# Performance work log

Measured on AMD Instinct MI355X. Metric: run time of the kernel, lower is better.

Reference implementation:

```python
import jax, jax.numpy as jnp
import numpy as np


def setup_inputs() -> dict:
    key = jax.random.key(0)
    ks = jax.random.split(key, 5)
    B, C, H, W = 4, 256, 64, 64
    Cq = C // 8
    x = jax.random.normal(ks[0], (B, C, H, W), dtype=jnp.float32)
    Wq = jax.random.normal(ks[1], (Cq, C), dtype=jnp.float32) * (1.0 / np.sqrt(C))
    Wk = jax.random.normal(ks[2], (Cq, C), dtype=jnp.float32) * (1.0 / np.sqrt(C))
    Wv = jax.random.normal(ks[3], (C, C), dtype=jnp.float32) * (1.0 / np.sqrt(C))
    bq = jnp.zeros((Cq,), dtype=jnp.float32)
    bk = jnp.zeros((Cq,), dtype=jnp.float32)
    bv = jnp.zeros((C,), dtype=jnp.float32)
    gamma = jnp.ones((1,), dtype=jnp.float32)
    return {"x": x, "Wq": Wq, "bq": bq, "Wk": Wk, "bk": bk, "Wv": Wv, "bv": bv, "gamma": gamma}


def reference(x, Wq, bq, Wk, bk, Wv, bv, gamma):
    B, C, H, W = x.shape
    N = H * W
    xf = x.reshape(B, C, N)                      # (B, C, N)
    # 1x1 convs == per-pixel linear projections over channels
    q = jnp.einsum('dc,bcn->bdn', Wq, xf) + bq[None, :, None]   # (B, C/8, N)
    k = jnp.einsum('dc,bcn->bdn', Wk, xf) + bk[None, :, None]   # (B, C/8, N)
    v = jnp.einsum('dc,bcn->bdn', Wv, xf) + bv[None, :, None]   # (B, C,   N)
    # attention: note original has NO 1/sqrt(d) scaling
    scores = jnp.einsum('bdn,bdm->bnm', q, k)     # (B, N, N)
    attn = jax.nn.softmax(scores, axis=-1)
    out = jnp.einsum('bnm,bdm->bnd', attn, v)     # (B, N, C)
    out = out.transpose(0, 2, 1).reshape(B, C, H, W)
    return gamma * out + x
```

## Files before the change

### kernel.cpp

```cpp
#include <hip/hip_runtime.h>

#define BATCH 4
#define CH    256
#define DQ    32
#define NPIX  4096

typedef unsigned short u16;
typedef unsigned int   u32;
typedef __attribute__((ext_vector_type(8))) short short8;
typedef __attribute__((ext_vector_type(16))) float f32x16;

__device__ __forceinline__ float b2f(u32 u) {
  union { u32 i; float f; } v; v.i = (u & 0xffffu) << 16; return v.f;
}
__device__ __forceinline__ u16 f2b(float f) {
  union { float f; u32 i; } v; v.f = f;
  u32 x = v.i; x += 0x7fffu + ((x >> 16) & 1u);
  return (u16)(x >> 16);
}

__global__ __launch_bounds__(256) void proj(
    const float* __restrict__ x,
    const float* __restrict__ Wq, const float* __restrict__ bq,
    const float* __restrict__ Wk, const float* __restrict__ bk,
    const float* __restrict__ Wv, const float* __restrict__ bv,
    u16* __restrict__ q_t, u16* __restrict__ k_t, u16* __restrict__ v_swz)
{
  const int nt = blockIdx.x, jt = blockIdx.y, b = blockIdx.z;
  const int t = threadIdx.x;
  const int w = t >> 6, lane = t & 63, hl = lane >> 5, l31 = lane & 31;
  const int n0 = nt * 128;

  __shared__ u16 wls[2][16 * 2 * 32 * 8];
  __shared__ u16 xls[2][128 * 24];
  __shared__ float bias_s[32];

  const float* Wsrc; const float* bsrc; int jrow0;
  if (jt == 0)      { Wsrc = Wq; bsrc = bq; jrow0 = 0; }
  else if (jt == 1) { Wsrc = Wk; bsrc = bk; jrow0 = 0; }
  else              { Wsrc = Wv; bsrc = bv; jrow0 = (jt - 2) * 32; }

  for (int i = 0; i < 32; ++i) {
    const int flat = i * 256 + t;
    const int j = flat >> 8, e = flat & 255;
    const float v = Wsrc[(size_t)(jrow0 + j) * CH + e];
    const u16 hi = f2b(v);
    const u16 lo = f2b(v - b2f(hi));
    const int idx = (((e >> 4) * 2 + ((e >> 3) & 1)) * 32 + j) * 8 + (e & 7);
    wls[0][idx] = hi; wls[1][idx] = lo;
  }
  if (t < 32) bias_s[t] = bsrc[jrow0 + t];

  f32x16 acc;
  #pragma unroll
  for (int r = 0; r < 16; ++r) acc[r] = 0.f;

  const int nn = t & 127, esub = (t >> 7) * 8;
  for (int kk = 0; kk < 16; ++kk) {
    __syncthreads();
    #pragma unroll
    for (int i2 = 0; i2 < 4; ++i2) {
      const int el = esub + 2 * i2;
      const float v0 = x[((size_t)b * CH + kk * 16 + el    ) * NPIX + n0 + nn];
      const float v1 = x[((size_t)b * CH + kk * 16 + el + 1) * NPIX + n0 + nn];
      const u16 h0 = f2b(v0), h1 = f2b(v1);
      const u16 lo0 = f2b(v0 - b2f(h0)), lo1 = f2b(v1 - b2f(h1));
      *(u32*)&xls[0][nn * 24 + el] = (u32)h0 | ((u32)h1 << 16);
      *(u32*)&xls[1][nn * 24 + el] = (u32)lo0 | ((u32)lo1 << 16);
    }
    __syncthreads();
    const short8 wa_h = *(const short8*)&wls[0][((kk * 2 + hl) * 32 + l31) * 8];
    const short8 wa_l = *(const short8*)&wls[1][((kk * 2 + hl) * 32 + l31) * 8];
    const int nb = w * 32 + l31;
    const short8 xb_h = *(const short8*)&xls[0][nb * 24 + hl * 8];
    const short8 xb_l = *(const short8*)&xls[1][nb * 24 + hl * 8];
    acc = __builtin_amdgcn_mfma_f32_32x32x16_bf16(wa_h, xb_h, acc, 0, 0, 0);
    acc = __builtin_amdgcn_mfma_f32_32x32x16_bf16(wa_h, xb_l, acc, 0, 0, 0);
    acc = __builtin_amdgcn_mfma_f32_32x32x16_bf16(wa_l, xb_h, acc, 0, 0, 0);
  }

  #pragma unroll
  for (int r = 0; r < 16; ++r)
    acc[r] += bias_s[(r & 3) + 8 * (r >> 2) + 4 * hl];

  if (jt <= 1) {
    u16* dst = (jt == 0) ? q_t : k_t;
    const int n = n0 + w * 32 + l31;
    #pragma unroll
    for (int r2 = 0; r2 < 4; ++r2) {
      uint2 pk;
      pk.x = (u32)f2b(acc[4 * r2 + 0]) | ((u32)f2b(acc[4 * r2 + 1]) << 16);
      pk.y = (u32)f2b(acc[4 * r2 + 2]) | ((u32)f2b(acc[4 * r2 + 3]) << 16);
      *(uint2*)(dst + ((size_t)b * NPIX + n) * DQ + 4 * hl + 8 * r2) = pk;
    }
  } else {
    const int mc = nt * 4 + w;
    const int kc = (l31 >> 4) & 1, h3 = (l31 >> 3) & 1, j8 = l31 & 7;
    u16* dst = v_swz + (((((size_t)b * 128 + mc) * 8 + (jt - 2)) * 2 + kc) * 2 + h3) * 256 + j8;
    #pragma unroll
    for (int r = 0; r < 16; ++r) {
      const int c5 = (r & 3) + 8 * (r >> 2) + 4 * hl;
      dst[c5 * 8] = f2b(acc[r]);
    }
  }
}

__global__ __launch_bounds__(256, 2) void attn(
    const u16* __restrict__ q_t, const u16* __restrict__ k_t,
    const u16* __restrict__ v_swz, const float* __restrict__ x,
    const float* __restrict__ gamma, float* __restrict__ out)
{
  const int b = blockIdx.y, t = threadIdx.x;
  const int w = t >> 6, lane = t & 63, hl = lane >> 5, l31 = lane & 31;
  const int n0 = blockIdx.x * 32;

  __shared__ float cbuf[8192];
  __shared__ float lbuf[4][64];

  short8 qf[2];
  #pragma unroll
  for (int kd = 0; kd < 2; ++kd)
    qf[kd] = *(const short8*)(q_t + ((size_t)b * NPIX + n0 + l31) * DQ + kd * 16 + hl * 8);

  f32x16 acc[8];
  #pragma unroll
  for (int ct = 0; ct < 8; ++ct)
    #pragma unroll
    for (int r = 0; r < 16; ++r) acc[ct][r] = 0.f;
  float lrun = 0.f;

  for (int cc = 0; cc < 32; ++cc) {
    const int mc = w * 32 + cc;

    const short8 kf0 = *(const short8*)(k_t + ((size_t)b * NPIX + mc * 32 + l31) * DQ + hl * 8);
    const short8 kf1 = *(const short8*)(k_t + ((size_t)b * NPIX + mc * 32 + l31) * DQ + 16 + hl * 8);
    f32x16 st;
    #pragma unroll
    for (int r = 0; r < 16; ++r) st[r] = 0.f;
    st = __builtin_amdgcn_mfma_f32_32x32x16_bf16(kf0, qf[0], st, 0, 0, 0);
    st = __builtin_amdgcn_mfma_f32_32x32x16_bf16(kf1, qf[1], st, 0, 0, 0);

    u32 pk[4][2];
    #pragma unroll
    for (int g = 0; g < 4; ++g) {
      const float e0 = __expf(st[4 * g + 0]);
      const float e1 = __expf(st[4 * g + 1]);
      const float e2 = __expf(st[4 * g + 2]);
      const float e3 = __expf(st[4 * g + 3]);
      lrun += (e0 + e1) + (e2 + e3);
      pk[g][0] = (u32)f2b(e0) | ((u32)f2b(e1) << 16);
      pk[g][1] = (u32)f2b(e2) | ((u32)f2b(e3) << 16);
    }

    const size_t vbase = ((size_t)b * 128 + mc) * 8192;
    #pragma unroll
    for (int kc = 0; kc < 2; ++kc) {
      const u32 s0 = hl ? pk[2 * kc][0] : pk[2 * kc + 1][0];
      const u32 s1 = hl ? pk[2 * kc][1] : pk[2 * kc + 1][1];
      const u32 r0 = (u32)__shfl_xor((int)s0, 32);
      const u32 r1 = (u32)__shfl_xor((int)s1, 32);
      union { uint4 u; short8 s; } bu;
      bu.u.x = hl ? r0 : pk[2 * kc][0];
      bu.u.y = hl ? r1 : pk[2 * kc][1];
      bu.u.z = hl ? pk[2 * kc + 1][0] : r0;
      bu.u.w = hl ? pk[2 * kc + 1][1] : r1;
      #pragma unroll
      for (int ct = 0; ct < 8; ++ct) {
        const short8 av = *(const short8*)(v_swz + vbase + (size_t)(((ct * 2 + kc) * 2 + hl) * 256) + l31 * 8);
        acc[ct] = __builtin_amdgcn_mfma_f32_32x32x16_bf16(av, bu.s, acc[ct], 0, 0, 0);
      }
    }
  }

  lbuf[w][lane] = lrun;
  __syncthreads();
  for (int src = 1; src < 4; ++src) {
    if (w == src) {
      #pragma unroll
      for (int ct = 0; ct < 8; ++ct)
        #pragma unroll
        for (int r = 0; r < 16; ++r)
          cbuf[(ct * 16 + r) * 64 + lane] = acc[ct][r];
    }
    __syncthreads();
    if (w == 0) {
      #pragma unroll
      for (int ct = 0; ct < 8; ++ct)
        #pragma unroll
        for (int r = 0; r < 16; ++r)
          acc[ct][r] += cbuf[(ct * 16 + r) * 64 + lane];
    }
    __syncthreads();
  }

  if (w == 0) {
    float l = (lbuf[0][lane] + lbuf[1][lane]) + (lbuf[2][lane] + lbuf[3][lane]);
    l += __shfl_xor(l, 32);
    const float linv = 1.0f / l;
    const float g = gamma[0];
    #pragma unroll
    for (int ct = 0; ct < 8; ++ct)
      #pragma unroll
      for (int r = 0; r < 16; ++r) {
        const int c = ct * 32 + (r & 3) + 8 * (r >> 2) + 4 * hl;
        const size_t idx = ((size_t)b * CH + c) * NPIX + n0 + l31;
        out[idx] = g * acc[ct][r] * linv + x[idx];
      }
  }
}

extern "C" void kernel_launch(void* const* d_in, const int* in_sizes, int n_in,
                              void* d_out, int out_size, void* d_ws, size_t ws_size,
                              hipStream_t stream) {
  const float* x  = (const float*)d_in[0];
  const float* Wq = (const float*)d_in[1];
  const float* bq = (const float*)d_in[2];
  const float* Wk = (const float*)d_in[3];
  const float* bk = (const float*)d_in[4];
  const float* Wv = (const float*)d_in[5];
  const float* bv = (const float*)d_in[6];
  const float* gm = (const float*)d_in[7];
  float* out = (float*)d_out;

  const size_t qk_elems = (size_t)BATCH * NPIX * DQ;
  const size_t v_elems  = (size_t)BATCH * NPIX * CH;
  const size_t need = (2 * qk_elems + v_elems) * sizeof(u16);
  if (ws_size < need) return;

  u16* q_t   = (u16*)d_ws;
  u16* k_t   = q_t + qk_elems;
  u16* v_swz = k_t + qk_elems;

  proj<<<dim3(32, 10, BATCH), 256, 0, stream>>>(x, Wq, bq, Wk, bk, Wv, bv, q_t, k_t, v_swz);
  attn<<<dim3(NPIX / 32, BATCH), 256, 0, stream>>>(q_t, k_t, v_swz, x, gm, out);
}
```

Baseline: 162.5 us.

## Precompute split-bf16 weights and x tiles, pipeline QK scores in attention loop

Weight hi/lo bf16 splitting moves into a one-off wprep kernel writing to device globals, and x is pre-split and transposed by a new xprep kernel into the output buffer as scratch. The projection kernel then reads MFMA-ready fragments straight from global with no LDS or barriers, and uses two accumulators. The attention loop computes the next chunk's scores while exponentiating the current one, prefetches K two steps ahead, folds log2e into Wq so exp2 can be used, swaps halves with permlane32_swap, and raises wave priority around the PV MFMAs. The extra kernel launches and the round trip of x through global memory add traffic and launch overhead.

```diff
diff --git a/kernel.cpp b/kernel.cpp
--- a/kernel.cpp
+++ b/kernel.cpp
@@ -4,12 +4,16 @@
 #define CH    256
 #define DQ    32
 #define NPIX  4096
+#define LOG2E 1.44269504088896340736f
 
 typedef unsigned short u16;
 typedef unsigned int   u32;
 typedef __attribute__((ext_vector_type(8))) short short8;
 typedef __attribute__((ext_vector_type(16))) float f32x16;
 
+__device__ __align__(16) u16 g_wbf[10 * 2 * 8192];
+__device__ float g_bias[10 * 32];
+
 __device__ __forceinline__ float b2f(u32 u) {
   union { u32 i; float f; } v; v.i = (u & 0xffffu) << 16; return v.f;
 }
@@ -18,79 +22,133 @@
   u32 x = v.i; x += 0x7fffu + ((x >> 16) & 1u);
   return (u16)(x >> 16);
 }
-
-__global__ __launch_bounds__(256) void proj(
-    const float* __restrict__ x,
+__device__ __forceinline__ float fexp2(float x) {
+#if __has_builtin(__builtin_amdgcn_exp2f)
+  return __builtin_amdgcn_exp2f(x);
+#else
+  return __expf(x * 0.69314718055994530942f);
+#endif
+}
+
+__device__ __forceinline__ void half_swap(u32 a0, u32 a1, u32 b0, u32 b1,
+                                          int hl, uint4& o) {
+#if __has_builtin(__builtin_amdgcn_permlane32_swap)
+  const auto r0 = __builtin_amdgcn_permlane32_swap((int)a0, (int)b0, false, false);
+  const auto r1 = __builtin_amdgcn_permlane32_swap((int)a1, (int)b1, false, false);
+  o.x = (u32)r0[0]; o.y = (u32)r1[0]; o.z = (u32)r0[1]; o.w = (u32)r1[1];
+#else
+  const u32 s0 = hl ? a0 : b0;
+  const u32 s1 = hl ? a1 : b1;
+  const u32 r0 = (u32)__shfl_xor((int)s0, 32);
+  const u32 r1 = (u32)__shfl_xor((int)s1, 32);
+  o.x = hl ? r0 : a0; o.y = hl ? r1 : a1;
+  o.z = hl ? b0 : r0; o.w = hl ? b1 : r1;
+#endif
+}
+
+__global__ __launch_bounds__(256) void wprep(
     const float* __restrict__ Wq, const float* __restrict__ bq,
     const float* __restrict__ Wk, const float* __restrict__ bk,
-    const float* __restrict__ Wv, const float* __restrict__ bv,
+    const float* __restrict__ Wv, const float* __restrict__ bv)
+{
+  const int jt = blockIdx.x, t = threadIdx.x;
+  const float* Wsrc; const float* bsrc; int jrow0; float scale = 1.f;
+  if (jt == 0)      { Wsrc = Wq; bsrc = bq; jrow0 = 0; scale = LOG2E; }
+  else if (jt == 1) { Wsrc = Wk; bsrc = bk; jrow0 = 0; }
+  else              { Wsrc = Wv; bsrc = bv; jrow0 = (jt - 2) * 32; }
+
+  u16* wdst = g_wbf + (size_t)jt * 16384;
+  for (int i = 0; i < 32; ++i) {
+    const int flat = i * 256 + t;
+    const int j = flat >> 8, e = flat & 255;
+    const float v = Wsrc[(size_t)(jrow0 + j) * CH + e] * scale;
+    const u16 hi = f2b(v);
+    const u16 lo = f2b(v - b2f(hi));
+    const int idx = (((e >> 4) * 2 + ((e >> 3) & 1)) * 32 + j) * 8 + (e & 7);
+    wdst[idx] = hi; wdst[8192 + idx] = lo;
+  }
+  if (t < 32) g_bias[jt * 32 + t] = bsrc[jrow0 + t] * scale;
+}
+
+__global__ __launch_bounds__(256) void xprep(
+    const float* __restrict__ x, u16* __restrict__ xt_hi, u16* __restrict__ xt_lo)
+{
+  const int nt = blockIdx.x, kb4 = blockIdx.y * 4, b = blockIdx.z;
+  const int n0 = nt * 128, c0 = blockIdx.y * 64;
+  const int t = threadIdx.x;
+  __shared__ u32 xls[64][129];
+
+  const int tn = t & 127, cp = t >> 7;
+  for (int i = 0; i < 32; ++i) {
+    const int c = cp + 2 * i;
+    const float v = x[((size_t)b * CH + c0 + c) * NPIX + n0 + tn];
+    const u16 h = f2b(v);
+    const u16 l = f2b(v - b2f(h));
+    xls[c][tn] = (u32)h | ((u32)l << 16);
+  }
+  __syncthreads();
+
+  for (int rep = 0; rep < 4; ++rep) {
+    const int id = t + 256 * rep;
+    const int kkhl = id >> 7, n = id & 127;
+    union { short8 s; uint4 u; } vh, vl;
+    #pragma unroll
+    for (int j = 0; j < 8; ++j) {
+      const u32 p = xls[kkhl * 8 + j][n];
+      vh.s[j] = (short)(p & 0xffffu);
+      vl.s[j] = (short)(p >> 16);
+    }
+    const size_t o = ((((size_t)(b * 32 + nt) * 16 + kb4 + (kkhl >> 1)) * 2
+                       + (kkhl & 1)) * 128 + n) * 8;
+    *(uint4*)(xt_hi + o) = vh.u;
+    *(uint4*)(xt_lo + o) = vl.u;
+  }
+}
+
+__global__ __launch_bounds__(256, 4) void proj(
+    const u16* __restrict__ xt_hi, const u16* __restrict__ xt_lo,
     u16* __restrict__ q_t, u16* __restrict__ k_t, u16* __restrict__ v_swz)
 {
   const int nt = blockIdx.x, jt = blockIdx.y, b = blockIdx.z;
   const int t = threadIdx.x;
   const int w = t >> 6, lane = t & 63, hl = lane >> 5, l31 = lane & 31;
-  const int n0 = nt * 128;
-
-  __shared__ u16 wls[2][16 * 2 * 32 * 8];
-  __shared__ u16 xls[2][128 * 24];
-  __shared__ float bias_s[32];
-
-  const float* Wsrc; const float* bsrc; int jrow0;
-  if (jt == 0)      { Wsrc = Wq; bsrc = bq; jrow0 = 0; }
-  else if (jt == 1) { Wsrc = Wk; bsrc = bk; jrow0 = 0; }
-  else              { Wsrc = Wv; bsrc = bv; jrow0 = (jt - 2) * 32; }
-
-  for (int i = 0; i < 32; ++i) {
-    const int flat = i * 256 + t;
-    const int j = flat >> 8, e = flat & 255;
-    const float v = Wsrc[(size_t)(jrow0 + j) * CH + e];
-    const u16 hi = f2b(v);
-    const u16 lo = f2b(v - b2f(hi));
-    const int idx = (((e >> 4) * 2 + ((e >> 3) & 1)) * 32 + j) * 8 + (e & 7);
-    wls[0][idx] = hi; wls[1][idx] = lo;
-  }
-  if (t < 32) bias_s[t] = bsrc[jrow0 + t];
-
-  f32x16 acc;
-  #pragma unroll
-  for (int r = 0; r < 16; ++r) acc[r] = 0.f;
-
-  const int nn = t & 127, esub = (t >> 7) * 8;
+  const int nb = w * 32 + l31, n = nt * 128 + nb;
+
+  const u16* __restrict__ wb = g_wbf + (size_t)jt * 16384;
+  const size_t xtile = (size_t)(b * 32 + nt) * 16 * 2 * 128 * 8;
+  const u16* __restrict__ xh = xt_hi + xtile;
+  const u16* __restrict__ xl = xt_lo + xtile;
+
+  f32x16 acc1, acc2;
+  #pragma unroll
+  for (int r = 0; r < 16; ++r) { acc1[r] = 0.f; acc2[r] = 0.f; }
+
+  #pragma unroll
   for (int kk = 0; kk < 16; ++kk) {
-    __syncthreads();
-    #pragma unroll
-    for (int i2 = 0; i2 < 4; ++i2) {
-      const int el = esub + 2 * i2;
-      const float v0 = x[((size_t)b * CH + kk * 16 + el    ) * NPIX + n0 + nn];
-      const float v1 = x[((size_t)b * CH + kk * 16 + el + 1) * NPIX + n0 + nn];
-      const u16 h0 = f2b(v0), h1 = f2b(v1);
-      const u16 lo0 = f2b(v0 - b2f(h0)), lo1 = f2b(v1 - b2f(h1));
-      *(u32*)&xls[0][nn * 24 + el] = (u32)h0 | ((u32)h1 << 16);
-      *(u32*)&xls[1][nn * 24 + el] = (u32)lo0 | ((u32)lo1 << 16);
-    }
-    __syncthreads();
-    const short8 wa_h = *(const short8*)&wls[0][((kk * 2 + hl) * 32 + l31) * 8];
-    const short8 wa_l = *(const short8*)&wls[1][((kk * 2 + hl) * 32 + l31) * 8];
-    const int nb = w * 32 + l31;
-    const short8 xb_h = *(const short8*)&xls[0][nb * 24 + hl * 8];
-    const short8 xb_l = *(const short8*)&xls[1][nb * 24 + hl * 8];
-    acc = __builtin_amdgcn_mfma_f32_32x32x16_bf16(wa_h, xb_h, acc, 0, 0, 0);
-    acc = __builtin_amdgcn_mfma_f32_32x32x16_bf16(wa_h, xb_l, acc, 0, 0, 0);
-    acc = __builtin_amdgcn_mfma_f32_32x32x16_bf16(wa_l, xb_h, acc, 0, 0, 0);
-  }
-
+    const int aoff = ((kk * 2 + hl) * 32 + l31) * 8;
+    const short8 wah = *(const short8*)(wb + aoff);
+    const short8 wal = *(const short8*)(wb + 8192 + aoff);
+    const int boff = ((kk * 2 + hl) * 128 + nb) * 8;
+    const short8 xbh = *(const short8*)(xh + boff);
+    const short8 xbl = *(const short8*)(xl + boff);
+    acc1 = __builtin_amdgcn_mfma_f32_32x32x16_bf16(wah, xbh, acc1, 0, 0, 0);
+    acc2 = __builtin_amdgcn_mfma_f32_32x32x16_bf16(wah, xbl, acc2, 0, 0, 0);
+    acc2 = __builtin_amdgcn_mfma_f32_32x32x16_bf16(wal, xbh, acc2, 0, 0, 0);
+  }
+
+  f32x16 accv;
   #pragma unroll
   for (int r = 0; r < 16; ++r)
-    acc[r] += bias_s[(r & 3) + 8 * (r >> 2) + 4 * hl];
+    accv[r] = acc1[r] + acc2[r]
+            + g_bias[jt * 32 + (r & 3) + 8 * (r >> 2) + 4 * hl];
 
   if (jt <= 1) {
     u16* dst = (jt == 0) ? q_t : k_t;
-    const int n = n0 + w * 32 + l31;
     #pragma unroll
     for (int r2 = 0; r2 < 4; ++r2) {
       uint2 pk;
-      pk.x = (u32)f2b(acc[4 * r2 + 0]) | ((u32)f2b(acc[4 * r2 + 1]) << 16);
-      pk.y = (u32)f2b(acc[4 * r2 + 2]) | ((u32)f2b(acc[4 * r2 + 3]) << 16);
+      pk.x = (u32)f2b(accv[4 * r2 + 0]) | ((u32)f2b(accv[4 * r2 + 1]) << 16);
+      pk.y = (u32)f2b(accv[4 * r2 + 2]) | ((u32)f2b(accv[4 * r2 + 3]) << 16);
       *(uint2*)(dst + ((size_t)b * NPIX + n) * DQ + 4 * hl + 8 * r2) = pk;
     }
   } else {
@@ -100,7 +158,7 @@
     #pragma unroll
     for (int r = 0; r < 16; ++r) {
       const int c5 = (r & 3) + 8 * (r >> 2) + 4 * hl;
-      dst[c5 * 8] = f2b(acc[r]);
+      dst[c5 * 8] = f2b(accv[r]);
     }
   }
 }
@@ -129,46 +187,57 @@
     for (int r = 0; r < 16; ++r) acc[ct][r] = 0.f;
   float lrun = 0.f;
 
+  const u16* __restrict__ kb = k_t + (size_t)b * NPIX * DQ;
+
+  short8 kf0 = *(const short8*)(kb + ((w * 32) * 32 + l31) * DQ + hl * 8);
+  short8 kf1 = *(const short8*)(kb + ((w * 32) * 32 + l31) * DQ + 16 + hl * 8);
+  f32x16 st;
+  #pragma unroll
+  for (int r = 0; r < 16; ++r) st[r] = 0.f;
+  st = __builtin_amdgcn_mfma_f32_32x32x16_bf16(kf0, qf[0], st, 0, 0, 0);
+  st = __builtin_amdgcn_mfma_f32_32x32x16_bf16(kf1, qf[1], st, 0, 0, 0);
+  kf0 = *(const short8*)(kb + ((w * 32 + 1) * 32 + l31) * DQ + hl * 8);
+  kf1 = *(const short8*)(kb + ((w * 32 + 1) * 32 + l31) * DQ + 16 + hl * 8);
+
+  #pragma unroll 1
   for (int cc = 0; cc < 32; ++cc) {
     const int mc = w * 32 + cc;
-
-    const short8 kf0 = *(const short8*)(k_t + ((size_t)b * NPIX + mc * 32 + l31) * DQ + hl * 8);
-    const short8 kf1 = *(const short8*)(k_t + ((size_t)b * NPIX + mc * 32 + l31) * DQ + 16 + hl * 8);
-    f32x16 st;
+    const size_t vbase = ((size_t)b * 128 + mc) * 8192;
+
+    u32 pk[4][2];
+    #pragma unroll
+    for (int g = 0; g < 4; ++g) {
+      const float e0 = fexp2(st[4 * g + 0]);
+      const float e1 = fexp2(st[4 * g + 1]);
+      const float e2 = fexp2(st[4 * g + 2]);
+      const float e3 = fexp2(st[4 * g + 3]);
+      lrun += (e0 + e1) + (e2 + e3);
+      pk[g][0] = (u32)f2b(e0) | ((u32)f2b(e1) << 16);
+      pk[g][1] = (u32)f2b(e2) | ((u32)f2b(e3) << 16);
+    }
+
     #pragma unroll
     for (int r = 0; r < 16; ++r) st[r] = 0.f;
     st = __builtin_amdgcn_mfma_f32_32x32x16_bf16(kf0, qf[0], st, 0, 0, 0);
     st = __builtin_amdgcn_mfma_f32_32x32x16_bf16(kf1, qf[1], st, 0, 0, 0);
 
-    u32 pk[4][2];
-    #pragma unroll
-    for (int g = 0; g < 4; ++g) {
-      const float e0 = __expf(st[4 * g + 0]);
-      const float e1 = __expf(st[4 * g + 1]);
-      const float e2 = __expf(st[4 * g + 2]);
-      const float e3 = __expf(st[4 * g + 3]);
-      lrun += (e0 + e1) + (e2 + e3);
-      pk[g][0] = (u32)f2b(e0) | ((u32)f2b(e1) << 16);
-      pk[g][1] = (u32)f2b(e2) | ((u32)f2b(e3) << 16);
-    }
-
-    const size_t vbase = ((size_t)b * 128 + mc) * 8192;
+    {
+      const int mcp = w * 32 + ((cc < 30) ? cc + 2 : 31);
+      kf0 = *(const short8*)(kb + (mcp * 32 + l31) * DQ + hl * 8);
+      kf1 = *(const short8*)(kb + (mcp * 32 + l31) * DQ + 16 + hl * 8);
+    }
+
     #pragma unroll
     for (int kc = 0; kc < 2; ++kc) {
-      const u32 s0 = hl ? pk[2 * kc][0] : pk[2 * kc + 1][0];
-      const u32 s1 = hl ? pk[2 * kc][1] : pk[2 * kc + 1][1];
-      const u32 r0 = (u32)__shfl_xor((int)s0, 32);
-      const u32 r1 = (u32)__shfl_xor((int)s1, 32);
       union { uint4 u; short8 s; } bu;
-      bu.u.x = hl ? r0 : pk[2 * kc][0];
-      bu.u.y = hl ? r1 : pk[2 * kc][1];
-      bu.u.z = hl ? pk[2 * kc + 1][0] : r0;
-      bu.u.w = hl ? pk[2 * kc + 1][1] : r1;
+      half_swap(pk[2 * kc][0], pk[2 * kc][1], pk[2 * kc + 1][0], pk[2 * kc + 1][1], hl, bu.u);
+      __builtin_amdgcn_s_setprio(1);
       #pragma unroll
       for (int ct = 0; ct < 8; ++ct) {
         const short8 av = *(const short8*)(v_swz + vbase + (size_t)(((ct * 2 + kc) * 2 + hl) * 256) + l31 * 8);
         acc[ct] = __builtin_amdgcn_mfma_f32_32x32x16_bf16(av, bu.s, acc[ct], 0, 0, 0);
       }
+      __builtin_amdgcn_s_setprio(0);
     }
   }
 
@@ -231,6 +300,11 @@
   u16* k_t   = q_t + qk_elems;
   u16* v_swz = k_t + qk_elems;
 
-  proj<<<dim3(32, 10, BATCH), 256, 0, stream>>>(x, Wq, bq, Wk, bk, Wv, bv, q_t, k_t, v_swz);
+  u16* xt_hi = (u16*)d_out;
+  u16* xt_lo = xt_hi + (size_t)BATCH * NPIX * CH;
+
+  wprep<<<dim3(10), 256, 0, stream>>>(Wq, bq, Wk, bk, Wv, bv);
+  xprep<<<dim3(NPIX / 128, CH / 64, BATCH), 256, 0, stream>>>(x, xt_hi, xt_lo);
+  proj<<<dim3(32, 10, BATCH), 256, 0, stream>>>(xt_hi, xt_lo, q_t, k_t, v_swz);
   attn<<<dim3(NPIX / 32, BATCH), 256, 0, stream>>>(q_t, k_t, v_swz, x, gm, out);
 }
```

Result: slower. 186.9 us (+15.0%).
